# Kernel tuning notes

Measured on AMD Instinct MI355X. Metric: run time of the kernel, lower is better.

## Reference

```python
import jax, jax.numpy as jnp
import numpy as np

# Fixed average-trace buffer from the module (length 120)
AVG = jnp.asarray([0.0256,0.0823,0.1157,0.1315,0.1366,0.1369,0.1347,0.1308,0.1259,0.1205,0.1146,0.1086,0.1028,0.097,0.0913,0.0858,0.0805,0.0756,0.0708,0.0664,0.0623,0.0584,0.0549,0.0515,0.0485,0.0456,0.0429,0.0404,0.0381,0.036,0.034,0.0321,0.0304,0.0287,0.0272,0.0258,0.0245,0.0233,0.0222,0.0211,0.0201,0.0191,0.0182,0.0173,0.0165,0.0158,0.015,0.0143,0.0137,0.013,0.0125,0.0119,0.0114,0.0108,0.0104,0.0099,0.0095,0.0091,0.0087,0.0083,0.008,0.0077,0.0074,0.0071,0.0068,0.0065,0.0062,0.006,0.0058,0.0055,0.0053,0.005,0.0049,0.0047,0.0045,0.0044,0.0042,0.004,0.0039,0.0038,0.0036,0.0034,0.0033,0.0032,0.0031,0.003,0.0029,0.0028,0.0027,0.0026,0.0025,0.0024,0.0023,0.0022,0.0021,0.0021,0.002,0.0019,0.0018,0.0018,0.0017,0.0017,0.0016,0.0016,0.0015,0.0015,0.0014,0.0014,0.0013,0.0013,0.0013,0.0012,0.0012,0.0011,0.0011,0.0011,0.001,0.001,0.001,0.0009], dtype=jnp.float32)


def _lstm(x, w_ih, w_hh, b):
    """PyTorch-semantics single-layer LSTM. x: [N,T,D], w_ih: [4H,D], w_hh: [4H,H], b: [4H] (= b_ih + b_hh). Gate order i,f,g,o."""
    xp = jnp.einsum('ntd,gd->ntg', x, w_ih) + b  # precompute input projections: [N,T,4H]
    N = x.shape[0]
    H = w_hh.shape[1]
    h0 = jnp.zeros((N, H), x.dtype)

    def step(carry, xt):
        h, c = carry
        g = xt + h @ w_hh.T  # [N,4H]
        i, f, gg, o = jnp.split(g, 4, axis=-1)
        c = jax.nn.sigmoid(f) * c + jax.nn.sigmoid(i) * jnp.tanh(gg)
        h = jax.nn.sigmoid(o) * jnp.tanh(c)
        return (h, c), h

    _, hs = jax.lax.scan(step, (h0, h0), jnp.swapaxes(xp, 0, 1))  # hs: [T,N,H]
    return jnp.swapaxes(hs, 0, 1)  # [N,T,H]


def setup_inputs() -> dict:
    key = jax.random.key(0)
    ks = jax.random.split(key, 7)
    N, F, H = 32768, 12, 30
    s1 = 1.0 / float(np.sqrt(H))  # torch LSTM init: U(-1/sqrt(H), 1/sqrt(H))
    s2 = 1.0                      # second LSTM hidden=1 -> scale 1
    return {
        'features': jax.random.normal(ks[0], (N, F), jnp.float32),
        'w_ih1': jax.random.uniform(ks[1], (4 * H, F + 1), jnp.float32, -s1, s1),
        'w_hh1': jax.random.uniform(ks[2], (4 * H, H), jnp.float32, -s1, s1),
        'b1': jax.random.uniform(ks[3], (4 * H,), jnp.float32, -s1, s1),
        'w_ih2': jax.random.uniform(ks[4], (4, H), jnp.float32, -s2, s2),
        'w_hh2': jax.random.uniform(ks[5], (4, 1), jnp.float32, -s2, s2),
        'b2': jax.random.uniform(ks[6], (4,), jnp.float32, -s2, s2),
    }


def reference(features, w_ih1, w_hh1, b1, w_ih2, w_hh2, b2):
    N, F = features.shape
    T = AVG.shape[0]  # 120
    x = jnp.broadcast_to(features[:, None, :], (N, T, F))          # repeat features over time
    trace = jnp.broadcast_to(AVG[None, :, None], (N, T, 1))        # average trace channel
    x = jnp.concatenate([x, trace], axis=2)                        # [N,120,13]
    h1 = _lstm(x, w_ih1, w_hh1, b1)                                # [N,120,30]
    return _lstm(h1, w_ih2, w_hh2, b2)                             # [N,120,1]
```

## Files before the change

### kernel.cpp

```cpp
#include <hip/hip_runtime.h>

typedef __attribute__((ext_vector_type(8))) short bf16x8;
typedef __attribute__((ext_vector_type(4))) float f32x4;

#define LOG2E 1.44269504088896340736f

__device__ __constant__ float AVG_D[120] = {
    0.0256f,0.0823f,0.1157f,0.1315f,0.1366f,0.1369f,0.1347f,0.1308f,0.1259f,0.1205f,
    0.1146f,0.1086f,0.1028f,0.0970f,0.0913f,0.0858f,0.0805f,0.0756f,0.0708f,0.0664f,
    0.0623f,0.0584f,0.0549f,0.0515f,0.0485f,0.0456f,0.0429f,0.0404f,0.0381f,0.0360f,
    0.0340f,0.0321f,0.0304f,0.0287f,0.0272f,0.0258f,0.0245f,0.0233f,0.0222f,0.0211f,
    0.0201f,0.0191f,0.0182f,0.0173f,0.0165f,0.0158f,0.0150f,0.0143f,0.0137f,0.0130f,
    0.0125f,0.0119f,0.0114f,0.0108f,0.0104f,0.0099f,0.0095f,0.0091f,0.0087f,0.0083f,
    0.0080f,0.0077f,0.0074f,0.0071f,0.0068f,0.0065f,0.0062f,0.0060f,0.0058f,0.0055f,
    0.0053f,0.0050f,0.0049f,0.0047f,0.0045f,0.0044f,0.0042f,0.0040f,0.0039f,0.0038f,
    0.0036f,0.0034f,0.0033f,0.0032f,0.0031f,0.0030f,0.0029f,0.0028f,0.0027f,0.0026f,
    0.0025f,0.0024f,0.0023f,0.0022f,0.0021f,0.0021f,0.0020f,0.0019f,0.0018f,0.0018f,
    0.0017f,0.0017f,0.0016f,0.0016f,0.0015f,0.0015f,0.0014f,0.0014f,0.0013f,0.0013f,
    0.0013f,0.0012f,0.0012f,0.0011f,0.0011f,0.0011f,0.0010f,0.0010f,0.0010f,0.0009f
};

__device__ __forceinline__ float sig2(float x) {
    return __builtin_amdgcn_rcpf(1.0f + __builtin_amdgcn_exp2f(x));
}
__device__ __forceinline__ float tanh2(float x) {
    return fmaf(2.0f, __builtin_amdgcn_rcpf(1.0f + __builtin_amdgcn_exp2f(x)), -1.0f);
}
__device__ __forceinline__ unsigned short tb(float x) {
    return (unsigned short)(__float_as_uint(x) >> 16);
}
__device__ __forceinline__ float fb(unsigned short h) {
    return __uint_as_float(((unsigned)h) << 16);
}

__global__ void pack_weights(const float* __restrict__ w_ih1,
                             const float* __restrict__ w_hh1,
                             const float* __restrict__ b1,
                             const float* __restrict__ w_ih2,
                             const float* __restrict__ b2,
                             float* __restrict__ ws) {
    unsigned short* whi = (unsigned short*)ws;
    unsigned short* wlo = (unsigned short*)(ws + 2048);
    float* bconst = ws + 4096;
    float* wih1f  = ws + 4224;
    unsigned* avgpk = (unsigned*)(ws + 5760);
    const int tid = threadIdx.x;
    for (int idx = tid; idx < 4096; idx += 256) {
        const int T = idx >> 9, lane = (idx >> 3) & 63, j = idx & 7;
        const int r = 16 * T + (lane & 15);
        const int k = ((lane >> 4) & 3) * 8 + j;
        const int u = r >> 2, q = r & 3;
        const float sc = (q == 2) ? (-2.0f * LOG2E) : (-LOG2E);
        float v = 0.0f;
        if (u < 30) {
            if (k < 30)       v = w_hh1[(q * 30 + u) * 30 + k];
            else if (k == 30) v = w_ih1[(q * 30 + u) * 13 + 12];
        } else if (u == 30 && k < 30) {
            v = w_ih2[q * 30 + k];
        }
        v *= sc;
        const unsigned short hi = tb(v);
        whi[idx] = hi;
        wlo[idx] = tb(v - fb(hi));
    }
    for (int r = tid; r < 128; r += 256) {
        const int u = r >> 2, q = r & 3;
        const float sc = (q == 2) ? (-2.0f * LOG2E) : (-LOG2E);
        bconst[r] = sc * ((u < 30) ? b1[q * 30 + u] : ((u == 30) ? b2[q] : 0.0f));
    }
    for (int idx = tid; idx < 1536; idx += 256) {
        const int r = idx / 12, d = idx % 12;
        const int u = r >> 2, q = r & 3;
        const float sc = (q == 2) ? (-2.0f * LOG2E) : (-LOG2E);
        wih1f[idx] = (u < 30) ? sc * w_ih1[(q * 30 + u) * 13 + d] : 0.0f;
    }
    for (int t = tid; t < 121; t += 256) {
        const float a = (t < 120) ? AVG_D[t] : 0.0f;
        const unsigned short hi = tb(a);
        const unsigned short lo = tb(a - fb(hi));
        avgpk[t] = (unsigned)hi | ((unsigned)lo << 16);
    }
}

__global__ __launch_bounds__(128, 4)
void lstm_mfma_kernel(const float* __restrict__ feat,
                      const float* __restrict__ w_hh2,
                      const float* __restrict__ ws,
                      float* __restrict__ out) {
    __shared__ unsigned hx[2][32 * 17];
    __shared__ __align__(16) float out_s[16 * 124];

    const int tid  = threadIdx.x;
    const int lane = tid & 63;
    const int wr   = __builtin_amdgcn_readfirstlane(tid >> 6);
    const int s    = lane & 15;
    const int quad = lane >> 4;
    const int seq  = blockIdx.x * 16 + s;
    const unsigned* avgpk = (const unsigned*)(ws + 5760);

    for (int i = tid; i < 1088; i += 128) (&hx[0][0])[i] = 0u;
    __syncthreads();
    if (tid < 16) hx[0][30 * 17 + tid] = avgpk[0];

    bf16x8 Ahi[4], Alo[4];
    {
        const unsigned short* whi = (const unsigned short*)ws;
        const unsigned short* wlo = (const unsigned short*)(ws + 2048);
#pragma unroll
        for (int Tl = 0; Tl < 4; Tl++) {
            Ahi[Tl] = *(const bf16x8*)(whi + (4 * wr + Tl) * 512 + lane * 8);
            Alo[Tl] = *(const bf16x8*)(wlo + (4 * wr + Tl) * 512 + lane * 8);
        }
    }

    float f0[12];
    {
        const float4* fp = reinterpret_cast<const float4*>(feat + seq * 12);
        float4 A = fp[0], B = fp[1], C = fp[2];
        f0[0]=A.x; f0[1]=A.y; f0[2]=A.z; f0[3]=A.w;
        f0[4]=B.x; f0[5]=B.y; f0[6]=B.z; f0[7]=B.w;
        f0[8]=C.x; f0[9]=C.y; f0[10]=C.z; f0[11]=C.w;
    }
    f32x4 projb[4];
    {
        const float* bconst = ws + 4096;
        const float* wih1f  = ws + 4224;
#pragma unroll
        for (int Tl = 0; Tl < 4; Tl++) {
#pragma unroll
            for (int g = 0; g < 4; g++) {
                const int r = 64 * wr + 16 * Tl + 4 * quad + g;
                float acc = bconst[r];
#pragma unroll
                for (int d = 0; d < 12; d++) acc = fmaf(f0[d], wih1f[r * 12 + d], acc);
                projb[Tl][g] = acc;
            }
        }
    }

    float c1[4];
#pragma unroll
    for (int Tl = 0; Tl < 4; Tl++) c1[Tl] = 0.0f;
    float h2 = 0.0f, c2 = 0.0f;
    const float whs0 = -LOG2E * w_hh2[0];
    const float whs1 = -LOG2E * w_hh2[1];
    const float whs2 = -2.0f * LOG2E * w_hh2[2];
    const float whs3 = -LOG2E * w_hh2[3];

    __syncthreads();

#pragma unroll 1
    for (int t = 0; t <= 120; t++) {
        const unsigned* hb = hx[t & 1];
        unsigned*       hn = hx[(t & 1) ^ 1];

        unsigned r0[8];
#pragma unroll
        for (int j = 0; j < 8; j++) r0[j] = hb[(8 * quad + j) * 17 + s];
        union { int4 i; bf16x8 v; } ubh, ubl;
        ubh.i.x = (int)__builtin_amdgcn_perm(r0[1], r0[0], 0x05040100u);
        ubh.i.y = (int)__builtin_amdgcn_perm(r0[3], r0[2], 0x05040100u);
        ubh.i.z = (int)__builtin_amdgcn_perm(r0[5], r0[4], 0x05040100u);
        ubh.i.w = (int)__builtin_amdgcn_perm(r0[7], r0[6], 0x05040100u);
        ubl.i.x = (int)__builtin_amdgcn_perm(r0[1], r0[0], 0x07060302u);
        ubl.i.y = (int)__builtin_amdgcn_perm(r0[3], r0[2], 0x07060302u);
        ubl.i.z = (int)__builtin_amdgcn_perm(r0[5], r0[4], 0x07060302u);
        ubl.i.w = (int)__builtin_amdgcn_perm(r0[7], r0[6], 0x07060302u);
        const bf16x8 Bhi = ubh.v, Blo = ubl.v;

        f32x4 D[4];
#pragma unroll
        for (int Tl = 0; Tl < 4; Tl++)
            D[Tl] = __builtin_amdgcn_mfma_f32_16x16x32_bf16(Alo[Tl], Bhi, projb[Tl], 0, 0, 0);
#pragma unroll
        for (int Tl = 0; Tl < 4; Tl++)
            D[Tl] = __builtin_amdgcn_mfma_f32_16x16x32_bf16(Ahi[Tl], Blo, D[Tl], 0, 0, 0);
#pragma unroll
        for (int Tl = 0; Tl < 4; Tl++)
            D[Tl] = __builtin_amdgcn_mfma_f32_16x16x32_bf16(Ahi[Tl], Bhi, D[Tl], 0, 0, 0);

        if (t >= 1 && wr == 1 && quad == 2) {
            const float g0 = fmaf(h2, whs0, D[3][0]);
            const float g1 = fmaf(h2, whs1, D[3][1]);
            const float g2 = fmaf(h2, whs2, D[3][2]);
            const float g3 = fmaf(h2, whs3, D[3][3]);
            c2 = sig2(g1) * c2 + sig2(g0) * tanh2(g2);
            h2 = sig2(g3) * tanh2(c2 * (-2.0f * LOG2E));
            out_s[s * 124 + (t - 1)] = h2;
        }

        if (t < 120) {
#pragma unroll
            for (int Tl = 0; Tl < 4; Tl++) {
                const int u = 16 * wr + 4 * Tl + quad;
                if (u < 30) {
                    const float ck = sig2(D[Tl][1]) * c1[Tl] + sig2(D[Tl][0]) * tanh2(D[Tl][2]);
                    c1[Tl] = ck;
                    const float hk = sig2(D[Tl][3]) * tanh2(ck * (-2.0f * LOG2E));
                    const unsigned bits = __float_as_uint(hk);
                    const float rem = hk - __uint_as_float(bits & 0xffff0000u);
                    const unsigned lo = __float_as_uint(rem) >> 16;
                    hn[u * 17 + s] = (bits >> 16) | (lo << 16);
                }
            }
            if (wr == 1 && lane < 16) hn[30 * 17 + lane] = avgpk[t + 1];
        }

        __syncthreads();
    }

    float* outb = out + (size_t)blockIdx.x * 16 * 120;
#pragma unroll
    for (int it = 0; it < 4; it++) {
        const int fi = it * 128 + tid;
        if (fi < 480) {
            const int sq = fi / 30, j = fi % 30;
            const float4 v = *reinterpret_cast<const float4*>(&out_s[sq * 124 + j * 4]);
            *reinterpret_cast<float4*>(&outb[sq * 120 + j * 4]) = v;
        }
    }
}

extern "C" void kernel_launch(void* const* d_in, const int* in_sizes, int n_in,
                              void* d_out, int out_size, void* d_ws, size_t ws_size,
                              hipStream_t stream) {
    (void)in_sizes; (void)n_in; (void)out_size; (void)ws_size;
    const float* feat  = (const float*)d_in[0];
    const float* w_ih1 = (const float*)d_in[1];
    const float* w_hh1 = (const float*)d_in[2];
    const float* b1    = (const float*)d_in[3];
    const float* w_ih2 = (const float*)d_in[4];
    const float* w_hh2 = (const float*)d_in[5];
    const float* b2    = (const float*)d_in[6];
    float* ws  = (float*)d_ws;
    float* out = (float*)d_out;

    hipLaunchKernelGGL(pack_weights, dim3(1), dim3(256), 0, stream,
                       w_ih1, w_hh1, b1, w_ih2, b2, ws);
    hipLaunchKernelGGL(lstm_mfma_kernel, dim3(2048), dim3(128), 0, stream,
                       feat, w_hh2, ws, out);
}
```

Measured before the change: 269.7 us.

## Process two 16-sequence groups per block to share weights and barriers

Each block now handles 32 sequences as two interleaved 16-column groups, halving the grid. The register-resident weight fragments and each per-step barrier are shared across both groups, and the two independent MFMA chains give the scheduler more instruction-level parallelism to hide the latency of the serial recurrence. In exchange, register use roughly doubles, the launch bound drops to 2 blocks per CU, and there are half as many blocks in flight.

```diff
diff --git a/kernel.cpp b/kernel.cpp
--- a/kernel.cpp
+++ b/kernel.cpp
@@ -82,25 +82,24 @@
     }
 }
 
-__global__ __launch_bounds__(128, 4)
+__global__ __launch_bounds__(128, 2)
 void lstm_mfma_kernel(const float* __restrict__ feat,
                       const float* __restrict__ w_hh2,
                       const float* __restrict__ ws,
                       float* __restrict__ out) {
-    __shared__ unsigned hx[2][32 * 17];
-    __shared__ __align__(16) float out_s[16 * 124];
+    __shared__ unsigned hx[2][2][32 * 17];
+    __shared__ __align__(16) float out_s[32 * 124];
 
     const int tid  = threadIdx.x;
     const int lane = tid & 63;
     const int wr   = __builtin_amdgcn_readfirstlane(tid >> 6);
     const int s    = lane & 15;
     const int quad = lane >> 4;
-    const int seq  = blockIdx.x * 16 + s;
     const unsigned* avgpk = (const unsigned*)(ws + 5760);
 
-    for (int i = tid; i < 1088; i += 128) (&hx[0][0])[i] = 0u;
+    for (int i = tid; i < 2176; i += 128) (&hx[0][0][0])[i] = 0u;
     __syncthreads();
-    if (tid < 16) hx[0][30 * 17 + tid] = avgpk[0];
+    if (tid < 32) hx[0][tid >> 4][30 * 17 + (tid & 15)] = avgpk[0];
 
     bf16x8 Ahi[4], Alo[4];
     {
@@ -113,35 +112,36 @@
         }
     }
 
-    float f0[12];
-    {
-        const float4* fp = reinterpret_cast<const float4*>(feat + seq * 12);
-        float4 A = fp[0], B = fp[1], C = fp[2];
-        f0[0]=A.x; f0[1]=A.y; f0[2]=A.z; f0[3]=A.w;
-        f0[4]=B.x; f0[5]=B.y; f0[6]=B.z; f0[7]=B.w;
-        f0[8]=C.x; f0[9]=C.y; f0[10]=C.z; f0[11]=C.w;
-    }
-    f32x4 projb[4];
+    f32x4 projb[2][4];
     {
         const float* bconst = ws + 4096;
         const float* wih1f  = ws + 4224;
 #pragma unroll
-        for (int Tl = 0; Tl < 4; Tl++) {
-#pragma unroll
-            for (int g = 0; g < 4; g++) {
-                const int r = 64 * wr + 16 * Tl + 4 * quad + g;
-                float acc = bconst[r];
-#pragma unroll
-                for (int d = 0; d < 12; d++) acc = fmaf(f0[d], wih1f[r * 12 + d], acc);
-                projb[Tl][g] = acc;
+        for (int g = 0; g < 2; g++) {
+            const int seq = blockIdx.x * 32 + g * 16 + s;
+            const float4* fp = reinterpret_cast<const float4*>(feat + seq * 12);
+            float4 A = fp[0], B = fp[1], C = fp[2];
+            float f0[12] = { A.x,A.y,A.z,A.w, B.x,B.y,B.z,B.w, C.x,C.y,C.z,C.w };
+#pragma unroll
+            for (int Tl = 0; Tl < 4; Tl++) {
+#pragma unroll
+                for (int gg = 0; gg < 4; gg++) {
+                    const int r = 64 * wr + 16 * Tl + 4 * quad + gg;
+                    float acc = bconst[r];
+#pragma unroll
+                    for (int d = 0; d < 12; d++) acc = fmaf(f0[d], wih1f[r * 12 + d], acc);
+                    projb[g][Tl][gg] = acc;
+                }
             }
         }
     }
 
-    float c1[4];
-#pragma unroll
-    for (int Tl = 0; Tl < 4; Tl++) c1[Tl] = 0.0f;
-    float h2 = 0.0f, c2 = 0.0f;
+    float c1[2][4];
+#pragma unroll
+    for (int g = 0; g < 2; g++)
+#pragma unroll
+        for (int Tl = 0; Tl < 4; Tl++) c1[g][Tl] = 0.0f;
+    float h2[2] = {0.0f, 0.0f}, c2[2] = {0.0f, 0.0f};
     const float whs0 = -LOG2E * w_hh2[0];
     const float whs1 = -LOG2E * w_hh2[1];
     const float whs2 = -2.0f * LOG2E * w_hh2[2];
@@ -151,69 +151,88 @@
 
 #pragma unroll 1
     for (int t = 0; t <= 120; t++) {
-        const unsigned* hb = hx[t & 1];
-        unsigned*       hn = hx[(t & 1) ^ 1];
-
-        unsigned r0[8];
-#pragma unroll
-        for (int j = 0; j < 8; j++) r0[j] = hb[(8 * quad + j) * 17 + s];
-        union { int4 i; bf16x8 v; } ubh, ubl;
-        ubh.i.x = (int)__builtin_amdgcn_perm(r0[1], r0[0], 0x05040100u);
-        ubh.i.y = (int)__builtin_amdgcn_perm(r0[3], r0[2], 0x05040100u);
-        ubh.i.z = (int)__builtin_amdgcn_perm(r0[5], r0[4], 0x05040100u);
-        ubh.i.w = (int)__builtin_amdgcn_perm(r0[7], r0[6], 0x05040100u);
-        ubl.i.x = (int)__builtin_amdgcn_perm(r0[1], r0[0], 0x07060302u);
-        ubl.i.y = (int)__builtin_amdgcn_perm(r0[3], r0[2], 0x07060302u);
-        ubl.i.z = (int)__builtin_amdgcn_perm(r0[5], r0[4], 0x07060302u);
-        ubl.i.w = (int)__builtin_amdgcn_perm(r0[7], r0[6], 0x07060302u);
-        const bf16x8 Bhi = ubh.v, Blo = ubl.v;
-
-        f32x4 D[4];
-#pragma unroll
-        for (int Tl = 0; Tl < 4; Tl++)
-            D[Tl] = __builtin_amdgcn_mfma_f32_16x16x32_bf16(Alo[Tl], Bhi, projb[Tl], 0, 0, 0);
-#pragma unroll
-        for (int Tl = 0; Tl < 4; Tl++)
-            D[Tl] = __builtin_amdgcn_mfma_f32_16x16x32_bf16(Ahi[Tl], Blo, D[Tl], 0, 0, 0);
-#pragma unroll
-        for (int Tl = 0; Tl < 4; Tl++)
-            D[Tl] = __builtin_amdgcn_mfma_f32_16x16x32_bf16(Ahi[Tl], Bhi, D[Tl], 0, 0, 0);
+        const int buf = t & 1;
+
+        bf16x8 Bhi[2], Blo[2];
+#pragma unroll
+        for (int g = 0; g < 2; g++) {
+            const unsigned* hb = hx[buf][g];
+            unsigned r0[8];
+#pragma unroll
+            for (int j = 0; j < 8; j++) r0[j] = hb[(8 * quad + j) * 17 + s];
+            union { int4 i; bf16x8 v; } ubh, ubl;
+            ubh.i.x = (int)__builtin_amdgcn_perm(r0[1], r0[0], 0x05040100u);
+            ubh.i.y = (int)__builtin_amdgcn_perm(r0[3], r0[2], 0x05040100u);
+            ubh.i.z = (int)__builtin_amdgcn_perm(r0[5], r0[4], 0x05040100u);
+            ubh.i.w = (int)__builtin_amdgcn_perm(r0[7], r0[6], 0x05040100u);
+            ubl.i.x = (int)__builtin_amdgcn_perm(r0[1], r0[0], 0x07060302u);
+            ubl.i.y = (int)__builtin_amdgcn_perm(r0[3], r0[2], 0x07060302u);
+            ubl.i.z = (int)__builtin_amdgcn_perm(r0[5], r0[4], 0x07060302u);
+            ubl.i.w = (int)__builtin_amdgcn_perm(r0[7], r0[6], 0x07060302u);
+            Bhi[g] = ubh.v; Blo[g] = ubl.v;
+        }
+
+        f32x4 D[2][4];
+#pragma unroll
+        for (int g = 0; g < 2; g++)
+#pragma unroll
+            for (int Tl = 0; Tl < 4; Tl++)
+                D[g][Tl] = __builtin_amdgcn_mfma_f32_16x16x32_bf16(Alo[Tl], Bhi[g], projb[g][Tl], 0, 0, 0);
+#pragma unroll
+        for (int g = 0; g < 2; g++)
+#pragma unroll
+            for (int Tl = 0; Tl < 4; Tl++)
+                D[g][Tl] = __builtin_amdgcn_mfma_f32_16x16x32_bf16(Ahi[Tl], Blo[g], D[g][Tl], 0, 0, 0);
+#pragma unroll
+        for (int g = 0; g < 2; g++)
+#pragma unroll
+            for (int Tl = 0; Tl < 4; Tl++)
+                D[g][Tl] = __builtin_amdgcn_mfma_f32_16x16x32_bf16(Ahi[Tl], Bhi[g], D[g][Tl], 0, 0, 0);
 
         if (t >= 1 && wr == 1 && quad == 2) {
-            const float g0 = fmaf(h2, whs0, D[3][0]);
-            const float g1 = fmaf(h2, whs1, D[3][1]);
-            const float g2 = fmaf(h2, whs2, D[3][2]);
-            const float g3 = fmaf(h2, whs3, D[3][3]);
-            c2 = sig2(g1) * c2 + sig2(g0) * tanh2(g2);
-            h2 = sig2(g3) * tanh2(c2 * (-2.0f * LOG2E));
-            out_s[s * 124 + (t - 1)] = h2;
+#pragma unroll
+            for (int g = 0; g < 2; g++) {
+                const float g0 = fmaf(h2[g], whs0, D[g][3][0]);
+                const float g1 = fmaf(h2[g], whs1, D[g][3][1]);
+                const float g2 = fmaf(h2[g], whs2, D[g][3][2]);
+                const float g3 = fmaf(h2[g], whs3, D[g][3][3]);
+                c2[g] = sig2(g1) * c2[g] + sig2(g0) * tanh2(g2);
+                h2[g] = sig2(g3) * tanh2(c2[g] * (-2.0f * LOG2E));
+                out_s[(g * 16 + s) * 124 + (t - 1)] = h2[g];
+            }
         }
 
         if (t < 120) {
 #pragma unroll
-            for (int Tl = 0; Tl < 4; Tl++) {
-                const int u = 16 * wr + 4 * Tl + quad;
-                if (u < 30) {
-                    const float ck = sig2(D[Tl][1]) * c1[Tl] + sig2(D[Tl][0]) * tanh2(D[Tl][2]);
-                    c1[Tl] = ck;
-                    const float hk = sig2(D[Tl][3]) * tanh2(ck * (-2.0f * LOG2E));
-                    const unsigned bits = __float_as_uint(hk);
-                    const float rem = hk - __uint_as_float(bits & 0xffff0000u);
-                    const unsigned lo = __float_as_uint(rem) >> 16;
-                    hn[u * 17 + s] = (bits >> 16) | (lo << 16);
+            for (int g = 0; g < 2; g++) {
+                unsigned* hn = hx[buf ^ 1][g];
+#pragma unroll
+                for (int Tl = 0; Tl < 4; Tl++) {
+                    const int u = 16 * wr + 4 * Tl + quad;
+                    if (u < 30) {
+                        const float ck = sig2(D[g][Tl][1]) * c1[g][Tl]
+                                       + sig2(D[g][Tl][0]) * tanh2(D[g][Tl][2]);
+                        c1[g][Tl] = ck;
+                        const float hk = sig2(D[g][Tl][3]) * tanh2(ck * (-2.0f * LOG2E));
+                        const unsigned bits = __float_as_uint(hk);
+                        const float rem = hk - __uint_as_float(bits & 0xffff0000u);
+                        const unsigned lo = __float_as_uint(rem) >> 16;
+                        hn[u * 17 + s] = (bits >> 16) | (lo << 16);
+                    }
                 }
             }
-            if (wr == 1 && lane < 16) hn[30 * 17 + lane] = avgpk[t + 1];
+            if (wr == 1 && lane < 32)
+                hx[buf ^ 1][lane >> 4][30 * 17 + (lane & 15)] = avgpk[t + 1];
         }
 
         __syncthreads();
     }
 
-    float* outb = out + (size_t)blockIdx.x * 16 * 120;
-#pragma unroll
-    for (int it = 0; it < 4; it++) {
+    float* outb = out + (size_t)blockIdx.x * 32 * 120;
+#pragma unroll
+    for (int it = 0; it < 8; it++) {
         const int fi = it * 128 + tid;
-        if (fi < 480) {
+        if (fi < 960) {
             const int sq = fi / 30, j = fi % 30;
             const float4 v = *reinterpret_cast<const float4*>(&out_s[sq * 124 + j * 4]);
             *reinterpret_cast<float4*>(&outb[sq * 120 + j * 4]) = v;
@@ -237,6 +256,6 @@
 
     hipLaunchKernelGGL(pack_weights, dim3(1), dim3(256), 0, stream,
                        w_ih1, w_hh1, b1, w_ih2, b2, ws);
-    hipLaunchKernelGGL(lstm_mfma_kernel, dim3(2048), dim3(128), 0, stream,
+    hipLaunchKernelGGL(lstm_mfma_kernel, dim3(1024), dim3(128), 0, stream,
                        feat, w_hh2, ws, out);
 }
```

After: 291.4 us. 8.1% more time.

## Transpose hidden-state LDS layout for vector reads and fuse gate reciprocals

Applied to the files above, without the earlier changes.

Changes the shared hidden-state buffer from unit-major (stride 17) to sequence-major (stride 36), so each lane fetches its eight packed hi/lo words with two 128-bit LDS loads instead of eight scalar loads. The LSTM cell math is rewritten to compute the four gate exponentials and then combine the sigmoid/tanh denominators algebraically, replacing several reciprocals with two. The cell argument is clamped before the exp, and the hi/lo bf16 packing uses a single byte-permute instruction. The intent is to shorten the serial per-timestep critical path (LDS reads plus transcendental/rcp count). The price is possible LDS bank conflicts on the strided writes and slightly different rounding, and the combined products could overflow for large gate values.

```diff
diff --git a/kernel.cpp b/kernel.cpp
--- a/kernel.cpp
+++ b/kernel.cpp
@@ -87,7 +87,7 @@
                       const float* __restrict__ w_hh2,
                       const float* __restrict__ ws,
                       float* __restrict__ out) {
-    __shared__ unsigned hx[2][32 * 17];
+    __shared__ __align__(16) unsigned hx[2][16 * 36];
     __shared__ __align__(16) float out_s[16 * 124];
 
     const int tid  = threadIdx.x;
@@ -98,9 +98,9 @@
     const int seq  = blockIdx.x * 16 + s;
     const unsigned* avgpk = (const unsigned*)(ws + 5760);
 
-    for (int i = tid; i < 1088; i += 128) (&hx[0][0])[i] = 0u;
+    for (int i = tid; i < 1152; i += 128) (&hx[0][0])[i] = 0u;
     __syncthreads();
-    if (tid < 16) hx[0][30 * 17 + tid] = avgpk[0];
+    if (tid < 16) hx[0][tid * 36 + 30] = avgpk[0];
 
     bf16x8 Ahi[4], Alo[4];
     {
@@ -151,21 +151,21 @@
 
 #pragma unroll 1
     for (int t = 0; t <= 120; t++) {
-        const unsigned* hb = hx[t & 1];
-        unsigned*       hn = hx[(t & 1) ^ 1];
-
-        unsigned r0[8];
-#pragma unroll
-        for (int j = 0; j < 8; j++) r0[j] = hb[(8 * quad + j) * 17 + s];
+        const int buf = t & 1;
+        const unsigned* hb = hx[buf];
+        unsigned*       hn = hx[buf ^ 1];
+
+        const uint4 Ra = *reinterpret_cast<const uint4*>(hb + s * 36 + 8 * quad);
+        const uint4 Rb = *reinterpret_cast<const uint4*>(hb + s * 36 + 8 * quad + 4);
         union { int4 i; bf16x8 v; } ubh, ubl;
-        ubh.i.x = (int)__builtin_amdgcn_perm(r0[1], r0[0], 0x05040100u);
-        ubh.i.y = (int)__builtin_amdgcn_perm(r0[3], r0[2], 0x05040100u);
-        ubh.i.z = (int)__builtin_amdgcn_perm(r0[5], r0[4], 0x05040100u);
-        ubh.i.w = (int)__builtin_amdgcn_perm(r0[7], r0[6], 0x05040100u);
-        ubl.i.x = (int)__builtin_amdgcn_perm(r0[1], r0[0], 0x07060302u);
-        ubl.i.y = (int)__builtin_amdgcn_perm(r0[3], r0[2], 0x07060302u);
-        ubl.i.z = (int)__builtin_amdgcn_perm(r0[5], r0[4], 0x07060302u);
-        ubl.i.w = (int)__builtin_amdgcn_perm(r0[7], r0[6], 0x07060302u);
+        ubh.i.x = (int)__builtin_amdgcn_perm(Ra.y, Ra.x, 0x05040100u);
+        ubh.i.y = (int)__builtin_amdgcn_perm(Ra.w, Ra.z, 0x05040100u);
+        ubh.i.z = (int)__builtin_amdgcn_perm(Rb.y, Rb.x, 0x05040100u);
+        ubh.i.w = (int)__builtin_amdgcn_perm(Rb.w, Rb.z, 0x05040100u);
+        ubl.i.x = (int)__builtin_amdgcn_perm(Ra.y, Ra.x, 0x07060302u);
+        ubl.i.y = (int)__builtin_amdgcn_perm(Ra.w, Ra.z, 0x07060302u);
+        ubl.i.z = (int)__builtin_amdgcn_perm(Rb.y, Rb.x, 0x07060302u);
+        ubl.i.w = (int)__builtin_amdgcn_perm(Rb.w, Rb.z, 0x07060302u);
         const bf16x8 Bhi = ubh.v, Blo = ubl.v;
 
         f32x4 D[4];
@@ -194,16 +194,28 @@
             for (int Tl = 0; Tl < 4; Tl++) {
                 const int u = 16 * wr + 4 * Tl + quad;
                 if (u < 30) {
-                    const float ck = sig2(D[Tl][1]) * c1[Tl] + sig2(D[Tl][0]) * tanh2(D[Tl][2]);
+                    const float ei = __builtin_amdgcn_exp2f(D[Tl][0]);
+                    const float ef = __builtin_amdgcn_exp2f(D[Tl][1]);
+                    const float eg = __builtin_amdgcn_exp2f(D[Tl][2]);
+                    const float eo = __builtin_amdgcn_exp2f(D[Tl][3]);
+                    const float pi_ = 1.0f + ei, pf = 1.0f + ef;
+                    const float pg  = 1.0f + eg, po = 1.0f + eo;
+                    const float pig = pi_ * pg;
+                    const float num = fmaf(c1[Tl], pig, (1.0f - eg) * pf);
+                    const float ck  = num * __builtin_amdgcn_rcpf(pf * pig);
                     c1[Tl] = ck;
-                    const float hk = sig2(D[Tl][3]) * tanh2(ck * (-2.0f * LOG2E));
-                    const unsigned bits = __float_as_uint(hk);
-                    const float rem = hk - __uint_as_float(bits & 0xffff0000u);
-                    const unsigned lo = __float_as_uint(rem) >> 16;
-                    hn[u * 17 + s] = (bits >> 16) | (lo << 16);
+                    float carg = -2.0f * LOG2E * ck;
+                    carg = fminf(fmaxf(carg, -80.0f), 80.0f);
+                    const float ec = __builtin_amdgcn_exp2f(carg);
+                    const float hk = (1.0f - ec) *
+                                     __builtin_amdgcn_rcpf(po * (1.0f + ec));
+                    const unsigned hbits = __float_as_uint(hk);
+                    const float rem = hk - __uint_as_float(hbits & 0xffff0000u);
+                    hn[s * 36 + u] = __builtin_amdgcn_perm(
+                        __float_as_uint(rem), hbits, 0x07060302u);
                 }
             }
-            if (wr == 1 && lane < 16) hn[30 * 17 + lane] = avgpk[t + 1];
+            if (wr == 1 && lane < 16) hn[lane * 36 + 30] = avgpk[t + 1];
         }
 
         __syncthreads();
```

New measurement: 257.5 us. 1.05x faster.
